# Performance work log

Hardware: AMD Instinct MI355X
Metric: run time of the kernel (lower is better)

Reference implementation:

```python
import jax, jax.numpy as jnp
import numpy as np

B, N, C = 8, 4096, 1024
ATT_DIM = 512
M = 64  # num_outputs


def setup_inputs() -> dict:
    key = jax.random.key(0)
    k_x, k_w, k_b, k_av = jax.random.split(key, 4)
    x = jax.random.normal(k_x, (B, N, C), dtype=jnp.float32)
    # nn.Linear(input_dim, attention_dim): weight (att, C), bias (att,)
    lim = 1.0 / np.sqrt(C)
    W = jax.random.uniform(k_w, (ATT_DIM, C), dtype=jnp.float32, minval=-lim, maxval=lim)
    b = jax.random.uniform(k_b, (ATT_DIM,), dtype=jnp.float32, minval=-lim, maxval=lim)
    # torch.rand -> uniform [0,1)
    attention_vectors = jax.random.uniform(k_av, (M, ATT_DIM), dtype=jnp.float32)
    return {"x": x, "W": W, "b": b, "attention_vectors": attention_vectors}


def reference(x, W, b, attention_vectors):
    # linear projection: (B,N,C) @ (C,att) + bias -> (B,N,att)
    scores = jnp.einsum('bnc,dc->bnd', x, W) + b
    # learned-query attention logits: (B,M,N)
    logits = jnp.einsum('bnd,md->bmn', scores, attention_vectors)
    weights = jax.nn.softmax(logits, axis=-1)
    # pool original features: (B,M,N) @ (B,N,C) -> (B,M,C)
    return jnp.einsum('bmn,bnc->bmc', weights, x)
```

## Files before the change

kernel.cpp:

```cpp
#include <hip/hip_runtime.h>
#include <hip/hip_bf16.h>

#define Bn 8
#define Nn 4096
#define Cn 1024
#define Dn 512
#define Mn 64

typedef __hip_bfloat16 bf16;
typedef __attribute__((ext_vector_type(8))) short short8;
typedef __attribute__((ext_vector_type(4))) short short4x;
typedef __attribute__((ext_vector_type(4))) float f32x4;

#define MFMA16(a, b, c) __builtin_amdgcn_mfma_f32_16x16x32_bf16((a), (b), (c), 0, 0, 0)

__device__ inline short bfbits(float f) {
  union { bf16 b; short s; } u;
  u.b = __float2bfloat16(f);
  return u.s;
}

__device__ __forceinline__ void gl_lds16(const bf16* g, short* l) {
  __builtin_amdgcn_global_load_lds(
      (const __attribute__((address_space(1))) void*)g,
      (__attribute__((address_space(3))) void*)l, 16, 0, 0);
}

__global__ __launch_bounds__(256) void prep_kernel(
    const float* __restrict__ W, const float* __restrict__ bias,
    const float* __restrict__ av, bf16* __restrict__ VgH,
    bf16* __restrict__ VgL, float* __restrict__ c0) {
  const int m = blockIdx.x;
  const int t = threadIdx.x;
  const int cl = t & 63, dg = t >> 6;
  const int c = blockIdx.y * 64 + cl;
  const float* wp = W + (size_t)(dg * 128) * Cn + c;
  const float* ap = av + m * Dn + dg * 128;
  float a0 = 0.f, a1 = 0.f, a2 = 0.f, a3 = 0.f;
#pragma unroll 8
  for (int i = 0; i < 128; i += 4) {
    a0 = fmaf(ap[i + 0], wp[(size_t)(i + 0) * Cn], a0);
    a1 = fmaf(ap[i + 1], wp[(size_t)(i + 1) * Cn], a1);
    a2 = fmaf(ap[i + 2], wp[(size_t)(i + 2) * Cn], a2);
    a3 = fmaf(ap[i + 3], wp[(size_t)(i + 3) * Cn], a3);
  }
  __shared__ float red[256];
  red[t] = (a0 + a1) + (a2 + a3);
  __syncthreads();
  const float v = red[cl] + red[cl + 64] + red[cl + 128] + red[cl + 192];
  if (dg == 0) {
    const int idx = blockIdx.y * 4096 + m * 64 + (cl ^ ((m & 7) << 3));
    const bf16 hi = __float2bfloat16(v);
    VgH[idx] = hi;
    VgL[idx] = __float2bfloat16(v - __bfloat162float(hi));
  }
  if (blockIdx.y == 0) {
    __syncthreads();
    red[t] = av[m * Dn + t] * bias[t] + av[m * Dn + t + 256] * bias[t + 256];
    __syncthreads();
    if (t < 64) {
      float s = red[t] + red[t + 64] + red[t + 128] + red[t + 192];
#pragma unroll
      for (int off = 32; off > 0; off >>= 1) s += __shfl_down(s, off);
      if (t == 0) c0[m] = s;
    }
  }
}

__global__ __launch_bounds__(256, 2) void logits_kernel(
    const float* __restrict__ x, const bf16* __restrict__ VgH,
    const bf16* __restrict__ VgL, const float* __restrict__ c0,
    float* __restrict__ logits) {
  const int n0 = blockIdx.x * 64;
  const int b = blockIdx.y;
  const int t = threadIdx.x;
  __shared__ short VsH[2][4096];
  __shared__ short VsL[2][4096];
  const int w = t >> 6, lane = t & 63, lr = lane & 15, q = lane >> 4;

  const float* xrow = x + (size_t)(b * Nn + n0 + w * 16 + lr) * Cn + q * 8;

  f32x4 acc[4];
#pragma unroll
  for (int i = 0; i < 4; ++i) acc[i] = (f32x4){0.f, 0.f, 0.f, 0.f};

#pragma unroll
  for (int r = 0; r < 2; ++r) {
    const int off = (w + 4 * r) * 512;
    gl_lds16(VgH + off + lane * 8, &VsH[0][off]);
    gl_lds16(VgL + off + lane * 8, &VsL[0][off]);
  }

  float4 xa0[2], xa1[2], xb0[2], xb1[2], xc0[2], xc1[2];
#pragma unroll
  for (int s = 0; s < 2; ++s) {
    xa0[s] = *(const float4*)(xrow + s * 32);
    xa1[s] = *(const float4*)(xrow + s * 32 + 4);
    xb0[s] = *(const float4*)(xrow + 64 + s * 32);
    xb1[s] = *(const float4*)(xrow + 64 + s * 32 + 4);
    xc0[s] = xb0[s]; xc1[s] = xb1[s];
  }

  const int rsw = (lr & 7) << 3;
  int cur = 0;
  for (int ck = 0; ck < 16; ++ck, cur ^= 1) {
    __syncthreads();
    if (ck + 1 < 16) {
#pragma unroll
      for (int r = 0; r < 2; ++r) {
        const int off = (w + 4 * r) * 512;
        gl_lds16(VgH + (ck + 1) * 4096 + off + lane * 8, &VsH[cur ^ 1][off]);
        gl_lds16(VgL + (ck + 1) * 4096 + off + lane * 8, &VsL[cur ^ 1][off]);
      }
    }
    const int kc = ck * 64;
    if (kc + 128 < Cn) {
#pragma unroll
      for (int s = 0; s < 2; ++s) {
        xc0[s] = *(const float4*)(xrow + kc + 128 + s * 32);
        xc1[s] = *(const float4*)(xrow + kc + 128 + s * 32 + 4);
      }
    }
#pragma unroll
    for (int s = 0; s < 2; ++s) {
      short8 a;
      a[0] = bfbits(xa0[s].x); a[1] = bfbits(xa0[s].y);
      a[2] = bfbits(xa0[s].z); a[3] = bfbits(xa0[s].w);
      a[4] = bfbits(xa1[s].x); a[5] = bfbits(xa1[s].y);
      a[6] = bfbits(xa1[s].z); a[7] = bfbits(xa1[s].w);
      const int kx = (s * 32 + q * 8) ^ rsw;
#pragma unroll
      for (int mt = 0; mt < 4; ++mt) {
        const int idx = (mt * 16 + lr) * 64 + kx;
        acc[mt] = MFMA16(a, *(const short8*)&VsH[cur][idx], acc[mt]);
        acc[mt] = MFMA16(a, *(const short8*)&VsL[cur][idx], acc[mt]);
      }
    }
#pragma unroll
    for (int s = 0; s < 2; ++s) {
      xa0[s] = xb0[s]; xa1[s] = xb1[s];
      xb0[s] = xc0[s]; xb1[s] = xc1[s];
    }
  }
#pragma unroll
  for (int mt = 0; mt < 4; ++mt) {
    const int m = mt * 16 + lr;
    const float bb = c0[m];
    float4 o;
    o.x = acc[mt][0] + bb; o.y = acc[mt][1] + bb;
    o.z = acc[mt][2] + bb; o.w = acc[mt][3] + bb;
    *(float4*)&logits[(size_t)(b * Mn + m) * Nn + n0 + w * 16 + q * 4] = o;
  }
}

__global__ __launch_bounds__(256) void softmax_kernel(
    const float* __restrict__ logits, bf16* __restrict__ wgt) {
  const int row = blockIdx.x;
  const int b = row >> 6, m = row & 63;
  const int t = threadIdx.x;
  const float* L = logits + (size_t)row * Nn;
  float v[16];
  float mx = -3.4e38f;
#pragma unroll
  for (int i = 0; i < 16; ++i) {
    v[i] = L[t + 256 * i];
    mx = fmaxf(mx, v[i]);
  }
#pragma unroll
  for (int off = 32; off > 0; off >>= 1) mx = fmaxf(mx, __shfl_down(mx, off));
  __shared__ float sred[4];
  if ((t & 63) == 0) sred[t >> 6] = mx;
  __syncthreads();
  mx = fmaxf(fmaxf(sred[0], sred[1]), fmaxf(sred[2], sred[3]));
  float sum = 0.f;
#pragma unroll
  for (int i = 0; i < 16; ++i) {
    v[i] = __expf(v[i] - mx);
    sum += v[i];
  }
#pragma unroll
  for (int off = 32; off > 0; off >>= 1) sum += __shfl_down(sum, off);
  __syncthreads();
  if ((t & 63) == 0) sred[t >> 6] = sum;
  __syncthreads();
  const float inv = 1.f / (sred[0] + sred[1] + sred[2] + sred[3]);
  const int msw = (m & 7) << 4;
#pragma unroll
  for (int i = 0; i < 16; ++i) {
    const int n = t + 256 * i;
    const int idx = (b * 32 + (n >> 7)) * 8192 + m * 128 + ((n & 127) ^ msw);
    wgt[idx] = __float2bfloat16(v[i] * inv);
  }
}

__global__ __launch_bounds__(256, 2) void pool_kernel(
    const float* __restrict__ x, const bf16* __restrict__ wgt,
    float* __restrict__ part) {
  const int cbase = blockIdx.x * 64;
  const int b = blockIdx.y;
  const int ks = blockIdx.z;
  const int t = threadIdx.x;
  __shared__ short XT[2][64][128];
  __shared__ short Ws[2][8192];
  const int w = t >> 6, lane = t & 63, lr = lane & 15, q = lane >> 4;
  const int mh = (w & 1) * 32, ch = (w >> 1) * 32;
  f32x4 acc[2][2];
#pragma unroll
  for (int i = 0; i < 2; ++i)
#pragma unroll
    for (int j = 0; j < 2; ++j) acc[i][j] = (f32x4){0.f, 0.f, 0.f, 0.f};

  const int h = t & 15, g = t >> 4;
  const int hb = 4 * (h & 1);
  const int NQ = Nn / 4;
  const int kbase = ks * NQ;
  const int tile0 = b * 32 + ks * 8;
  const float* xsrc = x + (size_t)b * Nn * Cn + (size_t)(kbase + 4 * g) * Cn + cbase + 4 * h;

#pragma unroll
  for (int r = 0; r < 4; ++r) {
    const int off = (w + 4 * r) * 512;
    gl_lds16(wgt + (size_t)tile0 * 8192 + off + lane * 8, &Ws[0][off]);
  }

  float4 pf[8];
#pragma unroll
  for (int i = 0; i < 4; ++i) {
    pf[i]     = *(const float4*)(xsrc + (size_t)i * Cn);
    pf[4 + i] = *(const float4*)(xsrc + (size_t)(64 + i) * Cn);
  }
#pragma unroll
  for (int blk = 0; blk < 2; ++blk) {
    const float4 r0 = pf[blk * 4 + 0], r1 = pf[blk * 4 + 1];
    const float4 r2 = pf[blk * 4 + 2], r3 = pf[blk * 4 + 3];
    const int kb2 = blk * 64 + 4 * g;
    short4x v0, v1, v2, v3;
    v0[0] = bfbits(r0.x); v0[1] = bfbits(r1.x); v0[2] = bfbits(r2.x); v0[3] = bfbits(r3.x);
    v1[0] = bfbits(r0.y); v1[1] = bfbits(r1.y); v1[2] = bfbits(r2.y); v1[3] = bfbits(r3.y);
    v2[0] = bfbits(r0.z); v2[1] = bfbits(r1.z); v2[2] = bfbits(r2.z); v2[3] = bfbits(r3.z);
    v3[0] = bfbits(r0.w); v3[1] = bfbits(r1.w); v3[2] = bfbits(r2.w); v3[3] = bfbits(r3.w);
    *(short4x*)&XT[0][4 * h + 0][kb2 ^ ((hb + 0) << 4)] = v0;
    *(short4x*)&XT[0][4 * h + 1][kb2 ^ ((hb + 1) << 4)] = v1;
    *(short4x*)&XT[0][4 * h + 2][kb2 ^ ((hb + 2) << 4)] = v2;
    *(short4x*)&XT[0][4 * h + 3][kb2 ^ ((hb + 3) << 4)] = v3;
  }
#pragma unroll
  for (int i = 0; i < 4; ++i) {
    pf[i]     = *(const float4*)(xsrc + (size_t)(128 + i) * Cn);
    pf[4 + i] = *(const float4*)(xsrc + (size_t)(192 + i) * Cn);
  }

  const int asw = (lr & 7) << 4;
  int cur = 0;
  for (int kc = 0; kc < NQ; kc += 128, cur ^= 1) {
    __syncthreads();
    if (kc + 128 < NQ) {
#pragma unroll
      for (int r = 0; r < 4; ++r) {
        const int off = (w + 4 * r) * 512;
        gl_lds16(wgt + (size_t)(tile0 + (kc >> 7) + 1) * 8192 + off + lane * 8,
                 &Ws[cur ^ 1][off]);
      }
#pragma unroll
      for (int blk = 0; blk < 2; ++blk) {
        const float4 r0 = pf[blk * 4 + 0], r1 = pf[blk * 4 + 1];
        const float4 r2 = pf[blk * 4 + 2], r3 = pf[blk * 4 + 3];
        const int kb2 = blk * 64 + 4 * g;
        short4x v0, v1, v2, v3;
        v0[0] = bfbits(r0.x); v0[1] = bfbits(r1.x); v0[2] = bfbits(r2.x); v0[3] = bfbits(r3.x);
        v1[0] = bfbits(r0.y); v1[1] = bfbits(r1.y); v1[2] = bfbits(r2.y); v1[3] = bfbits(r3.y);
        v2[0] = bfbits(r0.z); v2[1] = bfbits(r1.z); v2[2] = bfbits(r2.z); v2[3] = bfbits(r3.z);
        v3[0] = bfbits(r0.w); v3[1] = bfbits(r1.w); v3[2] = bfbits(r2.w); v3[3] = bfbits(r3.w);
        *(short4x*)&XT[cur ^ 1][4 * h + 0][kb2 ^ ((hb + 0) << 4)] = v0;
        *(short4x*)&XT[cur ^ 1][4 * h + 1][kb2 ^ ((hb + 1) << 4)] = v1;
        *(short4x*)&XT[cur ^ 1][4 * h + 2][kb2 ^ ((hb + 2) << 4)] = v2;
        *(short4x*)&XT[cur ^ 1][4 * h + 3][kb2 ^ ((hb + 3) << 4)] = v3;
      }
      if (kc + 256 < NQ) {
#pragma unroll
        for (int i = 0; i < 4; ++i) {
          pf[i]     = *(const float4*)(xsrc + (size_t)(kc + 256 + i) * Cn);
          pf[4 + i] = *(const float4*)(xsrc + (size_t)(kc + 320 + i) * Cn);
        }
      }
    }
#pragma unroll
    for (int kk = 0; kk < 128; kk += 32) {
      const int kx = (kk + q * 8) ^ asw;
      const short8 a0 = *(const short8*)&Ws[cur][(mh + lr) * 128 + kx];
      const short8 a1 = *(const short8*)&Ws[cur][(mh + 16 + lr) * 128 + kx];
      const short8 b0 = *(const short8*)&XT[cur][ch + lr][kx];
      const short8 b1 = *(const short8*)&XT[cur][ch + 16 + lr][kx];
      acc[0][0] = MFMA16(a0, b0, acc[0][0]);
      acc[0][1] = MFMA16(a0, b1, acc[0][1]);
      acc[1][0] = MFMA16(a1, b0, acc[1][0]);
      acc[1][1] = MFMA16(a1, b1, acc[1][1]);
    }
  }
  float* pout = part + ((size_t)ks * Bn + b) * Mn * Cn;
#pragma unroll
  for (int mi = 0; mi < 2; ++mi)
#pragma unroll
    for (int ci = 0; ci < 2; ++ci) {
      const int m = mh + mi * 16 + q * 4;
      const int c = cbase + ch + ci * 16 + lr;
#pragma unroll
      for (int reg = 0; reg < 4; ++reg)
        pout[(size_t)(m + reg) * Cn + c] = acc[mi][ci][reg];
    }
}

__global__ __launch_bounds__(256) void reduce_kernel(
    const float* __restrict__ part, float* __restrict__ out) {
  const int i = blockIdx.x * 256 + threadIdx.x;
  const float4* p = (const float4*)part;
  const int S4 = (Bn * Mn * Cn) / 4;
  float4 o = (float4){0.f, 0.f, 0.f, 0.f};
#pragma unroll
  for (int j = 0; j < 4; ++j) {
    const float4 v = p[i + j * S4];
    o.x += v.x; o.y += v.y; o.z += v.z; o.w += v.w;
  }
  ((float4*)out)[i] = o;
}

extern "C" void kernel_launch(void* const* d_in, const int* in_sizes, int n_in,
                              void* d_out, int out_size, void* d_ws, size_t ws_size,
                              hipStream_t stream) {
  const float* x = (const float*)d_in[0];
  const float* W = (const float*)d_in[1];
  const float* bias = (const float*)d_in[2];
  const float* av = (const float*)d_in[3];
  float* out = (float*)d_out;
  char* ws = (char*)d_ws;

  bf16* VgH = (bf16*)(ws + 0);
  bf16* VgL = (bf16*)(ws + 131072);
  float* c0 = (float*)(ws + 262144);
  bf16* wgt = (bf16*)(ws + 263168);
  float* logits = (float*)(ws + 4457472);
  float* part = (float*)(ws + 4457472);

  prep_kernel<<<dim3(Mn, Cn / 64), 256, 0, stream>>>(W, bias, av, VgH, VgL, c0);
  logits_kernel<<<dim3(Nn / 64, Bn), 256, 0, stream>>>(x, VgH, VgL, c0, logits);
  softmax_kernel<<<Bn * Mn, 256, 0, stream>>>(logits, wgt);
  pool_kernel<<<dim3(Cn / 64, Bn, 4), 256, 0, stream>>>(x, wgt, part);
  reduce_kernel<<<(Bn * Mn * Cn) / 1024, 256, 0, stream>>>(part, out);
}
```

Before: 256.3 us.

## Pre-swizzle V into MFMA fragment order and read directly from global

```diff
diff --git a/kernel.cpp b/kernel.cpp
--- a/kernel.cpp
+++ b/kernel.cpp
@@ -28,8 +28,8 @@
 
 __global__ __launch_bounds__(256) void prep_kernel(
     const float* __restrict__ W, const float* __restrict__ bias,
-    const float* __restrict__ av, bf16* __restrict__ VgH,
-    bf16* __restrict__ VgL, float* __restrict__ c0) {
+    const float* __restrict__ av, short* __restrict__ Vf,
+    float* __restrict__ c0) {
   const int m = blockIdx.x;
   const int t = threadIdx.x;
   const int cl = t & 63, dg = t >> 6;
@@ -49,10 +49,15 @@
   __syncthreads();
   const float v = red[cl] + red[cl + 64] + red[cl + 128] + red[cl + 192];
   if (dg == 0) {
-    const int idx = blockIdx.y * 4096 + m * 64 + (cl ^ ((m & 7) << 3));
+    const int ks = c >> 5, q = (c >> 3) & 3, j = c & 7;
+    const int mt = m >> 4, lr = m & 15;
+    const int base = (ks * 8 + mt * 2) * 512 + (q * 16 + lr) * 8 + j;
     const bf16 hi = __float2bfloat16(v);
-    VgH[idx] = hi;
-    VgL[idx] = __float2bfloat16(v - __bfloat162float(hi));
+    union { bf16 b; short s; } uh, ul;
+    uh.b = hi;
+    ul.b = __float2bfloat16(v - __bfloat162float(hi));
+    Vf[base] = uh.s;
+    Vf[base + 512] = ul.s;
   }
   if (blockIdx.y == 0) {
     __syncthreads();
@@ -68,78 +73,35 @@
 }
 
 __global__ __launch_bounds__(256, 2) void logits_kernel(
-    const float* __restrict__ x, const bf16* __restrict__ VgH,
-    const bf16* __restrict__ VgL, const float* __restrict__ c0,
-    float* __restrict__ logits) {
+    const float* __restrict__ x, const short* __restrict__ Vf,
+    const float* __restrict__ c0, float* __restrict__ logits) {
   const int n0 = blockIdx.x * 64;
   const int b = blockIdx.y;
   const int t = threadIdx.x;
-  __shared__ short VsH[2][4096];
-  __shared__ short VsL[2][4096];
   const int w = t >> 6, lane = t & 63, lr = lane & 15, q = lane >> 4;
 
   const float* xrow = x + (size_t)(b * Nn + n0 + w * 16 + lr) * Cn + q * 8;
+  const short* vfl = Vf + lane * 8;
 
   f32x4 acc[4];
 #pragma unroll
   for (int i = 0; i < 4; ++i) acc[i] = (f32x4){0.f, 0.f, 0.f, 0.f};
 
 #pragma unroll
-  for (int r = 0; r < 2; ++r) {
-    const int off = (w + 4 * r) * 512;
-    gl_lds16(VgH + off + lane * 8, &VsH[0][off]);
-    gl_lds16(VgL + off + lane * 8, &VsL[0][off]);
-  }
-
-  float4 xa0[2], xa1[2], xb0[2], xb1[2], xc0[2], xc1[2];
-#pragma unroll
-  for (int s = 0; s < 2; ++s) {
-    xa0[s] = *(const float4*)(xrow + s * 32);
-    xa1[s] = *(const float4*)(xrow + s * 32 + 4);
-    xb0[s] = *(const float4*)(xrow + 64 + s * 32);
-    xb1[s] = *(const float4*)(xrow + 64 + s * 32 + 4);
-    xc0[s] = xb0[s]; xc1[s] = xb1[s];
-  }
-
-  const int rsw = (lr & 7) << 3;
-  int cur = 0;
-  for (int ck = 0; ck < 16; ++ck, cur ^= 1) {
-    __syncthreads();
-    if (ck + 1 < 16) {
-#pragma unroll
-      for (int r = 0; r < 2; ++r) {
-        const int off = (w + 4 * r) * 512;
-        gl_lds16(VgH + (ck + 1) * 4096 + off + lane * 8, &VsH[cur ^ 1][off]);
-        gl_lds16(VgL + (ck + 1) * 4096 + off + lane * 8, &VsL[cur ^ 1][off]);
-      }
-    }
-    const int kc = ck * 64;
-    if (kc + 128 < Cn) {
-#pragma unroll
-      for (int s = 0; s < 2; ++s) {
-        xc0[s] = *(const float4*)(xrow + kc + 128 + s * 32);
-        xc1[s] = *(const float4*)(xrow + kc + 128 + s * 32 + 4);
-      }
-    }
-#pragma unroll
-    for (int s = 0; s < 2; ++s) {
-      short8 a;
-      a[0] = bfbits(xa0[s].x); a[1] = bfbits(xa0[s].y);
-      a[2] = bfbits(xa0[s].z); a[3] = bfbits(xa0[s].w);
-      a[4] = bfbits(xa1[s].x); a[5] = bfbits(xa1[s].y);
-      a[6] = bfbits(xa1[s].z); a[7] = bfbits(xa1[s].w);
-      const int kx = (s * 32 + q * 8) ^ rsw;
-#pragma unroll
-      for (int mt = 0; mt < 4; ++mt) {
-        const int idx = (mt * 16 + lr) * 64 + kx;
-        acc[mt] = MFMA16(a, *(const short8*)&VsH[cur][idx], acc[mt]);
-        acc[mt] = MFMA16(a, *(const short8*)&VsL[cur][idx], acc[mt]);
-      }
-    }
-#pragma unroll
-    for (int s = 0; s < 2; ++s) {
-      xa0[s] = xb0[s]; xa1[s] = xb1[s];
-      xb0[s] = xc0[s]; xb1[s] = xc1[s];
+  for (int ks = 0; ks < 32; ++ks) {
+    const float4 x0 = *(const float4*)(xrow + ks * 32);
+    const float4 x1 = *(const float4*)(xrow + ks * 32 + 4);
+    short8 a;
+    a[0] = bfbits(x0.x); a[1] = bfbits(x0.y);
+    a[2] = bfbits(x0.z); a[3] = bfbits(x0.w);
+    a[4] = bfbits(x1.x); a[5] = bfbits(x1.y);
+    a[6] = bfbits(x1.z); a[7] = bfbits(x1.w);
+#pragma unroll
+    for (int mt = 0; mt < 4; ++mt) {
+      const short8 vh = *(const short8*)(vfl + (ks * 8 + mt * 2) * 512);
+      const short8 vl = *(const short8*)(vfl + (ks * 8 + mt * 2 + 1) * 512);
+      acc[mt] = MFMA16(a, vh, acc[mt]);
+      acc[mt] = MFMA16(a, vl, acc[mt]);
     }
   }
 #pragma unroll
@@ -334,15 +296,14 @@
   float* out = (float*)d_out;
   char* ws = (char*)d_ws;
 
-  bf16* VgH = (bf16*)(ws + 0);
-  bf16* VgL = (bf16*)(ws + 131072);
+  short* Vf = (short*)(ws + 0);
   float* c0 = (float*)(ws + 262144);
   bf16* wgt = (bf16*)(ws + 263168);
   float* logits = (float*)(ws + 4457472);
   float* part = (float*)(ws + 4457472);
 
-  prep_kernel<<<dim3(Mn, Cn / 64), 256, 0, stream>>>(W, bias, av, VgH, VgL, c0);
-  logits_kernel<<<dim3(Nn / 64, Bn), 256, 0, stream>>>(x, VgH, VgL, c0, logits);
+  prep_kernel<<<dim3(Mn, Cn / 64), 256, 0, stream>>>(W, bias, av, Vf, c0);
+  logits_kernel<<<dim3(Nn / 64, Bn), 256, 0, stream>>>(x, Vf, c0, logits);
   softmax_kernel<<<Bn * Mn, 256, 0, stream>>>(logits, wgt);
   pool_kernel<<<dim3(Cn / 64, Bn, 4), 256, 0, stream>>>(x, wgt, part);
   reduce_kernel<<<(Bn * Mn * Cn) / 1024, 256, 0, stream>>>(part, out);
```

Result: slower. 264.7 us (+3.3%).
